# Kernel optimization log

Measured on AMD Instinct MI355X. Metric: run time of the kernel, lower is better.

Reference implementation:

```python
import jax, jax.numpy as jnp
import numpy as np

BS, CLS, C, H, W = 8, 4, 256, 128, 128
L, TK = 19, 256
MH, MW = 64, 64


def setup_inputs() -> dict:
    key = jax.random.key(0)
    ks = jax.random.split(key, 7)
    return {
        "mask_t": jax.random.uniform(ks[0], (BS, CLS, 1, MH, MW), dtype=jnp.float32),
        "fea_t": jax.random.normal(ks[1], (BS, C, H, W), dtype=jnp.float32),
        "token_s": jax.random.normal(ks[2], (BS, L, TK), dtype=jnp.float32),
        "W1": jax.random.normal(ks[3], (TK, C), dtype=jnp.float32) / np.sqrt(C),
        "W2": jax.random.normal(ks[4], (TK, TK), dtype=jnp.float32) / np.sqrt(TK),
        "W3": jax.random.normal(ks[5], (C, TK), dtype=jnp.float32) / np.sqrt(TK),
        "b3": jnp.zeros((C,), dtype=jnp.float32),
    }


def reference(mask_t, fea_t, token_s, W1, W2, W3, b3):
    bs, c, h, w = fea_t.shape
    cls = mask_t.shape[1]
    mh, mw = mask_t.shape[-2], mask_t.shape[-1]
    # F.interpolate nearest: out index i -> in index floor(i * in/out)
    ri = (jnp.arange(h) * mh) // h
    ci = (jnp.arange(w) * mw) // w
    m = mask_t.reshape(bs * cls, 1, mh, mw)[:, :, ri][:, :, :, ci]  # [bs*cls,1,h,w]
    # replicate torch's fea_t.repeat(cls,1,1,1) ordering (copy-major: index c*bs+b)
    # then the product is re-viewed batch-major (b*cls+c): fea index = (b*cls+cl) % bs
    idx = jnp.arange(bs * cls) % bs
    fea_c = (fea_t[idx] * m).reshape(bs, cls, c, h, w).mean(axis=1)  # [bs,c,h,w]
    q = fea_c.reshape(bs, c, h * w).transpose(0, 2, 1)  # [bs, HW, C]
    # forward_cell
    x_q = jnp.einsum('bnc,tc->bnt', q, W1)            # [bs,HW,TK]
    t_q = jnp.einsum('blc,tc->blt', token_s, W2)      # [bs,L,TK]
    a = jnp.einsum('bnt,blt->bnl', x_q, t_q)          # [bs,HW,L]
    a_soft = jax.nn.softmax(a / jnp.sqrt(jnp.float32(c)), axis=2)
    # sparse nonzero round-trip == zero out positions where logits are exactly 0
    a_soft = jnp.where(a != 0, a_soft, jnp.float32(0))
    t3 = jnp.einsum('blt,ot->blo', token_s, W3) + b3  # [bs,L,out]
    out = jnp.einsum('bnl,blo->bno', a_soft, t3)      # [bs,HW,out]
    out = out.transpose(0, 2, 1).reshape(bs, c, h, w)
    return out + fea_t
```

## Files before the change

kernel.cpp:

```cpp
#include <hip/hip_runtime.h>
#include <math.h>

#define BS   8
#define CLS  4
#define CCH  256
#define HH   128
#define WW   128
#define HWSZ (HH * WW)
#define LL   19
#define TKK  256
#define MHH  64
#define MWW  64

__global__ __launch_bounds__(256) void k_prep(
    const float* __restrict__ token, const float* __restrict__ W1,
    const float* __restrict__ W2, const float* __restrict__ W3,
    const float* __restrict__ b3, float* __restrict__ u,
    float* __restrict__ t3t) {
  __shared__ float tok_s[TKK];
  __shared__ float tq_s[TKK];
  const int bl = blockIdx.x;
  const int b  = bl / LL;
  const int l  = bl - b * LL;
  const int t  = threadIdx.x;
  tok_s[t] = token[(size_t)bl * TKK + t];
  __syncthreads();
  const float4* w2r = (const float4*)(W2 + (size_t)t * TKK);
  const float4* w3r = (const float4*)(W3 + (size_t)t * TKK);
  float a2 = 0.f, a3 = 0.f;
#pragma unroll 8
  for (int i = 0; i < TKK / 4; ++i) {
    float4 x = w2r[i];
    float4 y = w3r[i];
    const float* ts = &tok_s[4 * i];
    a2 += x.x * ts[0] + x.y * ts[1] + x.z * ts[2] + x.w * ts[3];
    a3 += y.x * ts[0] + y.y * ts[1] + y.z * ts[2] + y.w * ts[3];
  }
  tq_s[t] = a2;
  t3t[((size_t)b * CCH + t) * 20 + l] = a3 + b3[t];
  __syncthreads();
  float s0 = 0.f, s1 = 0.f, s2 = 0.f, s3 = 0.f;
#pragma unroll 4
  for (int k = 0; k < TKK; k += 4) {
    s0 += W1[(k + 0) * CCH + t] * tq_s[k + 0];
    s1 += W1[(k + 1) * CCH + t] * tq_s[k + 1];
    s2 += W1[(k + 2) * CCH + t] * tq_s[k + 2];
    s3 += W1[(k + 3) * CCH + t] * tq_s[k + 3];
  }
  u[(size_t)bl * CCH + t] = (s0 + s1 + s2 + s3) * (1.0f / 64.0f);
}

__global__ __launch_bounds__(256, 2) void k_main(
    const float* __restrict__ mask, const float* __restrict__ fea,
    const float* __restrict__ u, const float* __restrict__ t3t,
    float* __restrict__ out) {
  __shared__ float u_s[LL][CCH];
  __shared__ float acc_s[LL][128];

  const int blk  = blockIdx.x;
  const int b    = blk & 7;
  const int tile = blk >> 3;
  const int n0   = tile * WW;
  const int t    = threadIdx.x;
  const int lane = t & 63;
  const int wv   = t >> 6;

#pragma unroll
  for (int l = 0; l < LL; ++l) u_s[l][t] = u[((size_t)b * LL + l) * CCH + t];
  for (int k = t; k < LL * 128; k += 256) ((float*)acc_s)[k] = 0.f;

  const int hrow = tile >> 1;
  const float m0 = mask[(((size_t)(b * CLS + 0)) * MHH + hrow) * MWW + lane];
  const float m1 = mask[(((size_t)(b * CLS + 1)) * MHH + hrow) * MWW + lane];
  const float m2 = mask[(((size_t)(b * CLS + 2)) * MHH + hrow) * MWW + lane];
  const float m3 = mask[(((size_t)(b * CLS + 3)) * MHH + hrow) * MWW + lane];

  __syncthreads();

  const int f0 = (b & 1) * 4;
  const float* fb0 = fea + (size_t)(f0 + 0) * CCH * HWSZ + n0;
  const float* fb1 = fea + (size_t)(f0 + 1) * CCH * HWSZ + n0;
  const float* fb2 = fea + (size_t)(f0 + 2) * CCH * HWSZ + n0;
  const float* fb3 = fea + (size_t)(f0 + 3) * CCH * HWSZ + n0;

  float facc[LL][2];
#pragma unroll
  for (int l = 0; l < LL; ++l) { facc[l][0] = 0.f; facc[l][1] = 0.f; }

  const int c0 = wv * 64;
#pragma unroll 2
  for (int cc = 0; cc < 64; cc += 4) {
    float2 q[4];
#pragma unroll
    for (int j = 0; j < 4; ++j) {
      const size_t coff = (size_t)(c0 + cc + j) * HWSZ;
      const float2 v0 = ((const float2*)(fb0 + coff))[lane];
      const float2 v1 = ((const float2*)(fb1 + coff))[lane];
      const float2 v2 = ((const float2*)(fb2 + coff))[lane];
      const float2 v3 = ((const float2*)(fb3 + coff))[lane];
      q[j].x = v0.x * m0 + v1.x * m1 + v2.x * m2 + v3.x * m3;
      q[j].y = v0.y * m0 + v1.y * m1 + v2.y * m2 + v3.y * m3;
    }
#pragma unroll
    for (int l = 0; l < LL; ++l) {
      const float4 uu = *(const float4*)&u_s[l][c0 + cc];
      facc[l][0] += q[0].x * uu.x + q[1].x * uu.y + q[2].x * uu.z + q[3].x * uu.w;
      facc[l][1] += q[0].y * uu.x + q[1].y * uu.y + q[2].y * uu.z + q[3].y * uu.w;
    }
  }

#pragma unroll
  for (int l = 0; l < LL; ++l) {
    atomicAdd(&acc_s[l][2 * lane + 0], facc[l][0]);
    atomicAdd(&acc_s[l][2 * lane + 1], facc[l][1]);
  }
  __syncthreads();

  if (t < 128) {
    float a[LL];
    float mx = -INFINITY;
#pragma unroll
    for (int l = 0; l < LL; ++l) { a[l] = acc_s[l][t]; mx = fmaxf(mx, a[l]); }
    float e[LL];
    float sum = 0.f;
#pragma unroll
    for (int l = 0; l < LL; ++l) { e[l] = __expf(a[l] - mx); sum += e[l]; }
    const float inv = 1.0f / sum;
#pragma unroll
    for (int l = 0; l < LL; ++l)
      acc_s[l][t] = (a[l] != 0.f) ? e[l] * inv : 0.f;
  }
  __syncthreads();

  float2 p[LL];
#pragma unroll
  for (int l = 0; l < LL; ++l) p[l] = *(const float2*)&acc_s[l][2 * lane];

  const int wvu = __builtin_amdgcn_readfirstlane(wv);
  const int ob  = wvu * 64;
#pragma unroll 4
  for (int i = 0; i < 64; ++i) {
    const int o = ob + i;
    const float* tr = t3t + ((size_t)b * CCH + o) * 20;
    float sx = 0.f, sy = 0.f;
#pragma unroll
    for (int l = 0; l < LL; ++l) {
      const float tv = tr[l];
      sx += p[l].x * tv;
      sy += p[l].y * tv;
    }
    const size_t off = ((size_t)b * CCH + o) * HWSZ + n0;
    const float2 r = ((const float2*)(fea + off))[lane];
    float2 res;
    res.x = sx + r.x;
    res.y = sy + r.y;
    ((float2*)(out + off))[lane] = res;
  }
}

extern "C" void kernel_launch(void* const* d_in, const int* in_sizes, int n_in,
                              void* d_out, int out_size, void* d_ws, size_t ws_size,
                              hipStream_t stream) {
  (void)in_sizes; (void)n_in; (void)out_size; (void)ws_size;
  const float* mask  = (const float*)d_in[0];
  const float* fea   = (const float*)d_in[1];
  const float* token = (const float*)d_in[2];
  const float* W1    = (const float*)d_in[3];
  const float* W2    = (const float*)d_in[4];
  const float* W3    = (const float*)d_in[5];
  const float* b3    = (const float*)d_in[6];
  float* out = (float*)d_out;

  float* u   = (float*)d_ws;
  float* t3t = u + BS * LL * CCH;

  k_prep<<<BS * LL, 256, 0, stream>>>(token, W1, W2, W3, b3, u, t3t);
  k_main<<<(HWSZ / WW) * BS, 256, 0, stream>>>(mask, fea, u, t3t, out);
}
```

Measured before the change: 371.6 us.

## Halve pixel tile per block, batch channel loads, stage t3 in LDS

The main kernel now handles 64 pixels per block instead of 128, which doubles the grid. Each lane holds one pixel with scalar loads, and 8 channels of all four feature batches are loaded together before the math, so more memory requests are in flight. The t3 matrix for the batch is copied into the shared buffer that held u, so the output stage reads it from LDS rather than through scalar global loads. Launch bounds rise to 3 blocks per SIMD. The risks are more register pressure and less contiguous access width per lane.

```diff
diff --git a/kernel.cpp b/kernel.cpp
--- a/kernel.cpp
+++ b/kernel.cpp
@@ -50,79 +50,84 @@
   u[(size_t)bl * CCH + t] = (s0 + s1 + s2 + s3) * (1.0f / 64.0f);
 }
 
-__global__ __launch_bounds__(256, 2) void k_main(
+__global__ __launch_bounds__(256, 3) void k_main(
     const float* __restrict__ mask, const float* __restrict__ fea,
     const float* __restrict__ u, const float* __restrict__ t3t,
     float* __restrict__ out) {
-  __shared__ float u_s[LL][CCH];
-  __shared__ float acc_s[LL][128];
+  __shared__ float4 sh_buf4[(CCH * 20) / 4];
+  __shared__ float acc_s[LL][64];
+  float* sh_buf = (float*)sh_buf4;
 
   const int blk  = blockIdx.x;
   const int b    = blk & 7;
-  const int tile = blk >> 3;
-  const int n0   = tile * WW;
+  const int s    = blk >> 3;
+  const int n0   = s * 64;
   const int t    = threadIdx.x;
   const int lane = t & 63;
   const int wv   = t >> 6;
 
 #pragma unroll
-  for (int l = 0; l < LL; ++l) u_s[l][t] = u[((size_t)b * LL + l) * CCH + t];
-  for (int k = t; k < LL * 128; k += 256) ((float*)acc_s)[k] = 0.f;
+  for (int l = 0; l < LL; ++l)
+    sh_buf[l * CCH + t] = u[((size_t)b * LL + l) * CCH + t];
+  for (int k = t; k < LL * 64; k += 256) ((float*)acc_s)[k] = 0.f;
 
-  const int hrow = tile >> 1;
-  const float m0 = mask[(((size_t)(b * CLS + 0)) * MHH + hrow) * MWW + lane];
-  const float m1 = mask[(((size_t)(b * CLS + 1)) * MHH + hrow) * MWW + lane];
-  const float m2 = mask[(((size_t)(b * CLS + 2)) * MHH + hrow) * MWW + lane];
-  const float m3 = mask[(((size_t)(b * CLS + 3)) * MHH + hrow) * MWW + lane];
+  const int mrow = s >> 2;
+  const int mcol = ((s & 1) << 5) + (lane >> 1);
+  const size_t mbase = ((size_t)(b * CLS) * MHH + mrow) * MWW + mcol;
+  const float m0 = mask[mbase];
+  const float m1 = mask[mbase + 1 * MHH * MWW];
+  const float m2 = mask[mbase + 2 * MHH * MWW];
+  const float m3 = mask[mbase + 3 * MHH * MWW];
 
   __syncthreads();
 
   const int f0 = (b & 1) * 4;
-  const float* fb0 = fea + (size_t)(f0 + 0) * CCH * HWSZ + n0;
-  const float* fb1 = fea + (size_t)(f0 + 1) * CCH * HWSZ + n0;
-  const float* fb2 = fea + (size_t)(f0 + 2) * CCH * HWSZ + n0;
-  const float* fb3 = fea + (size_t)(f0 + 3) * CCH * HWSZ + n0;
+  const float* fb = fea + (size_t)f0 * CCH * HWSZ + n0 + lane;
+  const int c0 = wv * 64;
 
-  float facc[LL][2];
+  float facc[LL];
 #pragma unroll
-  for (int l = 0; l < LL; ++l) { facc[l][0] = 0.f; facc[l][1] = 0.f; }
+  for (int l = 0; l < LL; ++l) facc[l] = 0.f;
 
-  const int c0 = wv * 64;
-#pragma unroll 2
-  for (int cc = 0; cc < 64; cc += 4) {
-    float2 q[4];
+  for (int cc = 0; cc < 64; cc += 8) {
+    const int c = c0 + cc;
+    float v0[8], v1[8], v2[8], v3[8];
 #pragma unroll
-    for (int j = 0; j < 4; ++j) {
-      const size_t coff = (size_t)(c0 + cc + j) * HWSZ;
-      const float2 v0 = ((const float2*)(fb0 + coff))[lane];
-      const float2 v1 = ((const float2*)(fb1 + coff))[lane];
-      const float2 v2 = ((const float2*)(fb2 + coff))[lane];
-      const float2 v3 = ((const float2*)(fb3 + coff))[lane];
-      q[j].x = v0.x * m0 + v1.x * m1 + v2.x * m2 + v3.x * m3;
-      q[j].y = v0.y * m0 + v1.y * m1 + v2.y * m2 + v3.y * m3;
+    for (int j = 0; j < 8; ++j) {
+      const size_t o0 = (size_t)(c + j) * HWSZ;
+      v0[j] = fb[o0];
+      v1[j] = fb[o0 + (size_t)1 * CCH * HWSZ];
+      v2[j] = fb[o0 + (size_t)2 * CCH * HWSZ];
+      v3[j] = fb[o0 + (size_t)3 * CCH * HWSZ];
     }
+    float q[8];
+#pragma unroll
+    for (int j = 0; j < 8; ++j)
+      q[j] = v0[j] * m0 + v1[j] * m1 + v2[j] * m2 + v3[j] * m3;
 #pragma unroll
     for (int l = 0; l < LL; ++l) {
-      const float4 uu = *(const float4*)&u_s[l][c0 + cc];
-      facc[l][0] += q[0].x * uu.x + q[1].x * uu.y + q[2].x * uu.z + q[3].x * uu.w;
-      facc[l][1] += q[0].y * uu.x + q[1].y * uu.y + q[2].y * uu.z + q[3].y * uu.w;
+      const float4 ua = *(const float4*)&sh_buf[l * CCH + c];
+      const float4 ub = *(const float4*)&sh_buf[l * CCH + c + 4];
+      facc[l] += q[0] * ua.x + q[1] * ua.y + q[2] * ua.z + q[3] * ua.w +
+                 q[4] * ub.x + q[5] * ub.y + q[6] * ub.z + q[7] * ub.w;
     }
   }
 
 #pragma unroll
-  for (int l = 0; l < LL; ++l) {
-    atomicAdd(&acc_s[l][2 * lane + 0], facc[l][0]);
-    atomicAdd(&acc_s[l][2 * lane + 1], facc[l][1]);
-  }
+  for (int l = 0; l < LL; ++l) atomicAdd(&acc_s[l][lane], facc[l]);
   __syncthreads();
 
-  if (t < 128) {
+  {
+    const float* t3b = t3t + (size_t)b * CCH * 20;
+    for (int k = t; k < CCH * 20; k += 256) sh_buf[k] = t3b[k];
+  }
+  if (t < 64) {
     float a[LL];
     float mx = -INFINITY;
 #pragma unroll
     for (int l = 0; l < LL; ++l) { a[l] = acc_s[l][t]; mx = fmaxf(mx, a[l]); }
+    float sum = 0.f;
     float e[LL];
-    float sum = 0.f;
 #pragma unroll
     for (int l = 0; l < LL; ++l) { e[l] = __expf(a[l] - mx); sum += e[l]; }
     const float inv = 1.0f / sum;
@@ -132,29 +137,32 @@
   }
   __syncthreads();
 
-  float2 p[LL];
+  float p[LL];
 #pragma unroll
-  for (int l = 0; l < LL; ++l) p[l] = *(const float2*)&acc_s[l][2 * lane];
+  for (int l = 0; l < LL; ++l) p[l] = acc_s[l][lane];
 
   const int wvu = __builtin_amdgcn_readfirstlane(wv);
   const int ob  = wvu * 64;
-#pragma unroll 4
-  for (int i = 0; i < 64; ++i) {
-    const int o = ob + i;
-    const float* tr = t3t + ((size_t)b * CCH + o) * 20;
-    float sx = 0.f, sy = 0.f;
+  const float* fres = fea + ((size_t)b * CCH + ob) * HWSZ + n0 + lane;
+  float*       ores = out + ((size_t)b * CCH + ob) * HWSZ + n0 + lane;
+
+  for (int i0 = 0; i0 < 64; i0 += 8) {
+    float r[8];
 #pragma unroll
-    for (int l = 0; l < LL; ++l) {
-      const float tv = tr[l];
-      sx += p[l].x * tv;
-      sy += p[l].y * tv;
+    for (int j = 0; j < 8; ++j) r[j] = fres[(size_t)(i0 + j) * HWSZ];
+#pragma unroll
+    for (int j = 0; j < 8; ++j) {
+      const int o = ob + i0 + j;
+      const float4* tv = (const float4*)&sh_buf[o * 20];
+      const float4 A = tv[0], B = tv[1], C = tv[2], D = tv[3], E = tv[4];
+      const float sres =
+          p[0]  * A.x + p[1]  * A.y + p[2]  * A.z + p[3]  * A.w +
+          p[4]  * B.x + p[5]  * B.y + p[6]  * B.z + p[7]  * B.w +
+          p[8]  * C.x + p[9]  * C.y + p[10] * C.z + p[11] * C.w +
+          p[12] * D.x + p[13] * D.y + p[14] * D.z + p[15] * D.w +
+          p[16] * E.x + p[17] * E.y + p[18] * E.z;
+      ores[(size_t)(i0 + j) * HWSZ] = sres + r[j];
     }
-    const size_t off = ((size_t)b * CCH + o) * HWSZ + n0;
-    const float2 r = ((const float2*)(fea + off))[lane];
-    float2 res;
-    res.x = sx + r.x;
-    res.y = sy + r.y;
-    ((float2*)(out + off))[lane] = res;
   }
 }
 
@@ -175,5 +183,5 @@
   float* t3t = u + BS * LL * CCH;
 
   k_prep<<<BS * LL, 256, 0, stream>>>(token, W1, W2, W3, b3, u, t3t);
-  k_main<<<(HWSZ / WW) * BS, 256, 0, stream>>>(mask, fea, u, t3t, out);
+  k_main<<<(HWSZ / 64) * BS, 256, 0, stream>>>(mask, fea, u, t3t, out);
 }
```

New measurement: 442.8 us. 19.2% more time.

## Split main kernel over eight waves and stage t3 in LDS; transpose prep weights

Applied to the files above, without the earlier changes.

The main kernel grows from 256 to 512 threads. Each wave now handles 32 channels instead of 64, both in the attention reduction and in the output projection. The per-batch t3 table is copied into shared memory, reusing the u buffer, so the output loop reads it with vector LDS loads instead of scalar global loads. Feature loads in that loop are also batched four at a time. A new kernel transposes W2 and W3 into workspace so the prep kernel's weight reads are coalesced, with the old prep kernel kept as a fallback when the workspace is too small. The launch bound of 512 threads with a minimum of 8 blocks may force a tight register budget and cause spills of the per-thread accumulators.

```diff
diff --git a/kernel.cpp b/kernel.cpp
--- a/kernel.cpp
+++ b/kernel.cpp
@@ -12,7 +12,69 @@
 #define MHH  64
 #define MWW  64
 
-__global__ __launch_bounds__(256) void k_prep(
+__global__ __launch_bounds__(256) void k_tr(
+    const float* __restrict__ W2, const float* __restrict__ W3,
+    float* __restrict__ W2T, float* __restrict__ W3T) {
+  __shared__ float tile[64][65];
+  const int blk = blockIdx.x;
+  const int m   = blk >> 4;
+  const int q   = blk & 15;
+  const int tr  = (q >> 2) * 64;
+  const int tc  = (q & 3) * 64;
+  const float* src = (m == 0) ? W2 : W3;
+  float*       dst = (m == 0) ? W2T : W3T;
+  const int t  = threadIdx.x;
+  const int c  = t & 63;
+  const int r0 = t >> 6;
+#pragma unroll
+  for (int rp = 0; rp < 64; rp += 4)
+    tile[rp + r0][c] = src[(size_t)(tr + rp + r0) * TKK + tc + c];
+  __syncthreads();
+#pragma unroll
+  for (int rp = 0; rp < 64; rp += 4)
+    dst[(size_t)(tc + rp + r0) * TKK + tr + c] = tile[c][rp + r0];
+}
+
+__global__ __launch_bounds__(256) void k_prep_tr(
+    const float* __restrict__ token, const float* __restrict__ W1,
+    const float* __restrict__ W2T, const float* __restrict__ W3T,
+    const float* __restrict__ b3, float* __restrict__ u,
+    float* __restrict__ t3t) {
+  __shared__ float tok_s[TKK];
+  __shared__ float tq_s[TKK];
+  const int bl = blockIdx.x;
+  const int b  = bl / LL;
+  const int l  = bl - b * LL;
+  const int t  = threadIdx.x;
+  tok_s[t] = token[(size_t)bl * TKK + t];
+  __syncthreads();
+  float a2a = 0.f, a2b = 0.f, a3a = 0.f, a3b = 0.f;
+#pragma unroll 8
+  for (int k = 0; k < TKK; k += 2) {
+    const float w2a = W2T[(size_t)(k + 0) * TKK + t];
+    const float w2b = W2T[(size_t)(k + 1) * TKK + t];
+    const float w3a = W3T[(size_t)(k + 0) * TKK + t];
+    const float w3b = W3T[(size_t)(k + 1) * TKK + t];
+    a2a += w2a * tok_s[k + 0];
+    a2b += w2b * tok_s[k + 1];
+    a3a += w3a * tok_s[k + 0];
+    a3b += w3b * tok_s[k + 1];
+  }
+  tq_s[t] = a2a + a2b;
+  t3t[((size_t)b * CCH + t) * 20 + l] = a3a + a3b + b3[t];
+  __syncthreads();
+  float s0 = 0.f, s1 = 0.f, s2 = 0.f, s3 = 0.f;
+#pragma unroll 8
+  for (int k = 0; k < TKK; k += 4) {
+    s0 += W1[(size_t)(k + 0) * CCH + t] * tq_s[k + 0];
+    s1 += W1[(size_t)(k + 1) * CCH + t] * tq_s[k + 1];
+    s2 += W1[(size_t)(k + 2) * CCH + t] * tq_s[k + 2];
+    s3 += W1[(size_t)(k + 3) * CCH + t] * tq_s[k + 3];
+  }
+  u[(size_t)bl * CCH + t] = (s0 + s1 + s2 + s3) * (1.0f / 64.0f);
+}
+
+__global__ __launch_bounds__(256) void k_prep_leg(
     const float* __restrict__ token, const float* __restrict__ W1,
     const float* __restrict__ W2, const float* __restrict__ W3,
     const float* __restrict__ b3, float* __restrict__ u,
@@ -50,12 +112,13 @@
   u[(size_t)bl * CCH + t] = (s0 + s1 + s2 + s3) * (1.0f / 64.0f);
 }
 
-__global__ __launch_bounds__(256, 2) void k_main(
+__global__ __launch_bounds__(512, 8) void k_main(
     const float* __restrict__ mask, const float* __restrict__ fea,
     const float* __restrict__ u, const float* __restrict__ t3t,
     float* __restrict__ out) {
-  __shared__ float u_s[LL][CCH];
+  __shared__ float4 sh_buf4[(CCH * 20) / 4];
   __shared__ float acc_s[LL][128];
+  float* sh_buf = (float*)sh_buf4;
 
   const int blk  = blockIdx.x;
   const int b    = blk & 7;
@@ -65,15 +128,16 @@
   const int lane = t & 63;
   const int wv   = t >> 6;
 
-#pragma unroll
-  for (int l = 0; l < LL; ++l) u_s[l][t] = u[((size_t)b * LL + l) * CCH + t];
-  for (int k = t; k < LL * 128; k += 256) ((float*)acc_s)[k] = 0.f;
+  for (int k = t; k < LL * CCH; k += 512)
+    sh_buf[k] = u[(size_t)b * LL * CCH + k];
+  for (int k = t; k < LL * 128; k += 512) ((float*)acc_s)[k] = 0.f;
 
   const int hrow = tile >> 1;
-  const float m0 = mask[(((size_t)(b * CLS + 0)) * MHH + hrow) * MWW + lane];
-  const float m1 = mask[(((size_t)(b * CLS + 1)) * MHH + hrow) * MWW + lane];
-  const float m2 = mask[(((size_t)(b * CLS + 2)) * MHH + hrow) * MWW + lane];
-  const float m3 = mask[(((size_t)(b * CLS + 3)) * MHH + hrow) * MWW + lane];
+  const size_t mbase = (((size_t)(b * CLS)) * MHH + hrow) * MWW + lane;
+  const float m0 = mask[mbase + (size_t)0 * MHH * MWW];
+  const float m1 = mask[mbase + (size_t)1 * MHH * MWW];
+  const float m2 = mask[mbase + (size_t)2 * MHH * MWW];
+  const float m3 = mask[mbase + (size_t)3 * MHH * MWW];
 
   __syncthreads();
 
@@ -87,9 +151,9 @@
 #pragma unroll
   for (int l = 0; l < LL; ++l) { facc[l][0] = 0.f; facc[l][1] = 0.f; }
 
-  const int c0 = wv * 64;
+  const int c0 = wv * 32;
 #pragma unroll 2
-  for (int cc = 0; cc < 64; cc += 4) {
+  for (int cc = 0; cc < 32; cc += 4) {
     float2 q[4];
 #pragma unroll
     for (int j = 0; j < 4; ++j) {
@@ -103,7 +167,7 @@
     }
 #pragma unroll
     for (int l = 0; l < LL; ++l) {
-      const float4 uu = *(const float4*)&u_s[l][c0 + cc];
+      const float4 uu = *(const float4*)&sh_buf[l * CCH + c0 + cc];
       facc[l][0] += q[0].x * uu.x + q[1].x * uu.y + q[2].x * uu.z + q[3].x * uu.w;
       facc[l][1] += q[0].y * uu.x + q[1].y * uu.y + q[2].y * uu.z + q[3].y * uu.w;
     }
@@ -116,6 +180,10 @@
   }
   __syncthreads();
 
+  {
+    const float* t3b = t3t + (size_t)b * CCH * 20;
+    for (int k = t; k < CCH * 20; k += 512) sh_buf[k] = t3b[k];
+  }
   if (t < 128) {
     float a[LL];
     float mx = -INFINITY;
@@ -137,31 +205,44 @@
   for (int l = 0; l < LL; ++l) p[l] = *(const float2*)&acc_s[l][2 * lane];
 
   const int wvu = __builtin_amdgcn_readfirstlane(wv);
-  const int ob  = wvu * 64;
-#pragma unroll 4
-  for (int i = 0; i < 64; ++i) {
-    const int o = ob + i;
-    const float* tr = t3t + ((size_t)b * CCH + o) * 20;
-    float sx = 0.f, sy = 0.f;
-#pragma unroll
-    for (int l = 0; l < LL; ++l) {
-      const float tv = tr[l];
-      sx += p[l].x * tv;
-      sy += p[l].y * tv;
-    }
-    const size_t off = ((size_t)b * CCH + o) * HWSZ + n0;
-    const float2 r = ((const float2*)(fea + off))[lane];
-    float2 res;
-    res.x = sx + r.x;
-    res.y = sy + r.y;
-    ((float2*)(out + off))[lane] = res;
+  const int ob  = wvu * 32;
+  for (int i0 = 0; i0 < 32; i0 += 4) {
+    float2 r[4];
+#pragma unroll
+    for (int j = 0; j < 4; ++j) {
+      const size_t off = ((size_t)b * CCH + ob + i0 + j) * HWSZ + n0;
+      r[j] = ((const float2*)(fea + off))[lane];
+    }
+#pragma unroll
+    for (int j = 0; j < 4; ++j) {
+      const int o = ob + i0 + j;
+      const float4* tv = (const float4*)&sh_buf[o * 20];
+      const float4 A = tv[0], B = tv[1], C = tv[2], D = tv[3], E = tv[4];
+      const float sx =
+          p[0].x  * A.x + p[1].x  * A.y + p[2].x  * A.z + p[3].x  * A.w +
+          p[4].x  * B.x + p[5].x  * B.y + p[6].x  * B.z + p[7].x  * B.w +
+          p[8].x  * C.x + p[9].x  * C.y + p[10].x * C.z + p[11].x * C.w +
+          p[12].x * D.x + p[13].x * D.y + p[14].x * D.z + p[15].x * D.w +
+          p[16].x * E.x + p[17].x * E.y + p[18].x * E.z;
+      const float sy =
+          p[0].y  * A.x + p[1].y  * A.y + p[2].y  * A.z + p[3].y  * A.w +
+          p[4].y  * B.x + p[5].y  * B.y + p[6].y  * B.z + p[7].y  * B.w +
+          p[8].y  * C.x + p[9].y  * C.y + p[10].y * C.z + p[11].y * C.w +
+          p[12].y * D.x + p[13].y * D.y + p[14].y * D.z + p[15].y * D.w +
+          p[16].y * E.x + p[17].y * E.y + p[18].y * E.z;
+      const size_t off = ((size_t)b * CCH + o) * HWSZ + n0;
+      float2 res;
+      res.x = sx + r[j].x;
+      res.y = sy + r[j].y;
+      ((float2*)(out + off))[lane] = res;
+    }
   }
 }
 
 extern "C" void kernel_launch(void* const* d_in, const int* in_sizes, int n_in,
                               void* d_out, int out_size, void* d_ws, size_t ws_size,
                               hipStream_t stream) {
-  (void)in_sizes; (void)n_in; (void)out_size; (void)ws_size;
+  (void)in_sizes; (void)n_in; (void)out_size;
   const float* mask  = (const float*)d_in[0];
   const float* fea   = (const float*)d_in[1];
   const float* token = (const float*)d_in[2];
@@ -173,7 +254,16 @@
 
   float* u   = (float*)d_ws;
   float* t3t = u + BS * LL * CCH;
-
-  k_prep<<<BS * LL, 256, 0, stream>>>(token, W1, W2, W3, b3, u, t3t);
-  k_main<<<(HWSZ / WW) * BS, 256, 0, stream>>>(mask, fea, u, t3t, out);
-}
+  float* W2T = t3t + BS * CCH * 20;
+  float* W3T = W2T + TKK * TKK;
+  const size_t ws_need =
+      (size_t)(BS * LL * CCH + BS * CCH * 20 + 2 * TKK * TKK) * sizeof(float);
+
+  if (ws_size >= ws_need) {
+    k_tr<<<32, 256, 0, stream>>>(W2, W3, W2T, W3T);
+    k_prep_tr<<<BS * LL, 256, 0, stream>>>(token, W1, W2T, W3T, b3, u, t3t);
+  } else {
+    k_prep_leg<<<BS * LL, 256, 0, stream>>>(token, W1, W2, W3, b3, u, t3t);
+  }
+  k_main<<<(HWSZ / WW) * BS, 512, 0, stream>>>(mask, fea, u, t3t, out);
+}
```

After: 556.5 us. 1.5x slower.
